# Kernel tuning notes

Measured on AMD Instinct MI355X. Metric: run time of the kernel, lower is better.

The kernel has to match this reference:

```python
import jax, jax.numpy as jnp
import numpy as np

N_HEADS = 8
D_MODEL = 512
HEAD_DIM = D_MODEL // N_HEADS


def setup_inputs() -> dict:
    key = jax.random.key(0)
    ks = jax.random.split(key, 9)
    B, T1, T2, D = 1, 4096, 4096, D_MODEL
    w_scale = 0.02
    return {
        "query": jax.random.normal(ks[0], (B, T1, D), dtype=jnp.float32),
        "key": jax.random.normal(ks[1], (B, T2, D), dtype=jnp.float32),
        "value": jax.random.normal(ks[2], (B, T2, D), dtype=jnp.float32),
        # True = padded (masked out); ~half positions masked
        "key_padding_mask": jax.random.randint(ks[3], (B, T2), 0, 2) == 1,
        "Wq_w": jax.random.normal(ks[4], (D, D), dtype=jnp.float32) * w_scale,
        "Wq_b": jnp.zeros((D,), dtype=jnp.float32),
        "Wk_w": jax.random.normal(ks[5], (D, D), dtype=jnp.float32) * w_scale,
        "Wk_b": jnp.zeros((D,), dtype=jnp.float32),
        "Wv_w": jax.random.normal(ks[6], (D, D), dtype=jnp.float32) * w_scale,
        "Wv_b": jnp.zeros((D,), dtype=jnp.float32),
        "Wo_w": jax.random.normal(ks[7], (D, D), dtype=jnp.float32) * w_scale,
        "Wo_b": jnp.zeros((D,), dtype=jnp.float32),
    }


def reference(query, key, value, key_padding_mask,
              Wq_w, Wq_b, Wk_w, Wk_b, Wv_w, Wv_b, Wo_w, Wo_b):
    B, T1, D = query.shape
    T2 = key.shape[1]
    H, HD = N_HEADS, HEAD_DIM

    # torch Linear: y = x @ W.T + b
    q = (query @ Wq_w.T + Wq_b).reshape(B, T1, H, HD).transpose(0, 2, 1, 3)  # [B,H,T1,HD]
    k = (key @ Wk_w.T + Wk_b).reshape(B, T2, H, HD).transpose(0, 2, 1, 3)    # [B,H,T2,HD]
    v = (value @ Wv_w.T + Wv_b).reshape(B, T2, H, HD).transpose(0, 2, 1, 3)  # [B,H,T2,HD]

    scale = 1.0 / (HD ** 0.5)
    scores = jnp.einsum("bhqd,bhkd->bhqk", q, k) * scale                     # [B,H,T1,T2]
    mask_value = jnp.finfo(scores.dtype).min
    scores = jnp.where(key_padding_mask[:, None, None, :], mask_value, scores)

    attn = jax.nn.softmax(scores, axis=-1)                                   # [B,H,T1,T2]
    # dropout p=0.0 (inference) -> identity

    out = jnp.einsum("bhqk,bhkd->bhqd", attn, v)                             # [B,H,T1,HD]
    out = out.transpose(0, 2, 1, 3).reshape(B, T1, D)
    out = out @ Wo_w.T + Wo_b
    return (out, attn)
```

## Files before the change

### kernel.cpp

```cpp
#include <hip/hip_runtime.h>
#include <hip/hip_bf16.h>
#include <float.h>
#include <stdint.h>

typedef __bf16 bf16x8 __attribute__((ext_vector_type(8)));
typedef __bf16 bf16x4 __attribute__((ext_vector_type(4)));
typedef float  f32x4  __attribute__((ext_vector_type(4)));

#define T_SEQ 4096
#define DMODEL 512
#define NH 8
#define HDIM 64
#define KS1 4
#define L2E 1.44269504088896340736f

__device__ __forceinline__ float fexp2(float x) { return __builtin_amdgcn_exp2f(x); }

__device__ __forceinline__ void gl_lds16(const __bf16* g, char* l) {
    __builtin_amdgcn_global_load_lds(
        (const __attribute__((address_space(1))) unsigned int*)(g),
        (__attribute__((address_space(3))) unsigned int*)(l),
        16, 0, 0);
}

__global__ __launch_bounds__(256) void qkv_kernel(
    const float* __restrict__ qin, const float* __restrict__ kin, const float* __restrict__ vin,
    const float* __restrict__ Wq, const float* __restrict__ bq,
    const float* __restrict__ Wk, const float* __restrict__ bk,
    const float* __restrict__ Wv, const float* __restrict__ bv,
    __bf16* __restrict__ qo, __bf16* __restrict__ ko, __bf16* __restrict__ vt)
{
    __shared__ char lds[16384];
    char* Ab = lds;
    char* Bb = lds + 8192;

    const int z = blockIdx.z;
    const float* X    = (z == 0) ? qin : (z == 1) ? kin : vin;
    const float* W    = (z == 0) ? Wq  : (z == 1) ? Wk  : Wv;
    const float* bias = (z == 0) ? bq  : (z == 1) ? bk  : bv;

    const int m0 = blockIdx.x * 64;
    const int n0 = blockIdx.y * 64;
    const int tid  = threadIdx.x;
    const int w    = tid >> 6;
    const int lane = tid & 63;
    const int lrow = lane & 15;
    const int lgrp = lane >> 4;

    f32x4 acc[4] = {};
    const int r  = tid >> 2;
    const int c0 = (tid & 3) * 16;

    for (int kt = 0; kt < 8; ++kt) {
        const int k0 = kt * 64;
        const float* gA = X + (size_t)(m0 + r) * DMODEL + k0 + c0;
        const float* gB = W + (size_t)(n0 + r) * DMODEL + k0 + c0;
        const int sw = (r & 7) << 4;
#pragma unroll
        for (int i = 0; i < 4; ++i) {
            float4 a4 = *(const float4*)(gA + 4 * i);
            float4 b4 = *(const float4*)(gB + 4 * i);
            bf16x4 av, bv4;
            av[0] = (__bf16)a4.x; av[1] = (__bf16)a4.y; av[2] = (__bf16)a4.z; av[3] = (__bf16)a4.w;
            bv4[0] = (__bf16)b4.x; bv4[1] = (__bf16)b4.y; bv4[2] = (__bf16)b4.z; bv4[3] = (__bf16)b4.w;
            *(bf16x4*)(Ab + r * 128 + ((c0 * 2 + 8 * i) ^ sw)) = av;
            *(bf16x4*)(Bb + r * 128 + ((c0 * 2 + 8 * i) ^ sw)) = bv4;
        }
        __syncthreads();
#pragma unroll
        for (int ks = 0; ks < 2; ++ks) {
            bf16x8 af = *(const bf16x8*)(Ab + (w * 16 + lrow) * 128 +
                                         ((ks * 64 + lgrp * 16) ^ ((lrow & 7) << 4)));
#pragma unroll
            for (int ns = 0; ns < 4; ++ns) {
                bf16x8 bf = *(const bf16x8*)(Bb + (ns * 16 + lrow) * 128 +
                                             ((ks * 64 + lgrp * 16) ^ ((lrow & 7) << 4)));
                acc[ns] = __builtin_amdgcn_mfma_f32_16x16x32_bf16(af, bf, acc[ns], 0, 0, 0);
            }
        }
        __syncthreads();
    }

    if (z == 2) {
        char* LT = lds;
#pragma unroll
        for (int ns = 0; ns < 4; ++ns) {
            float bcol = bias[n0 + ns * 16 + lrow];
#pragma unroll
            for (int rr = 0; rr < 4; ++rr) {
                int col = ns * 16 + lrow;
                int row = w * 16 + lgrp * 4 + rr;
                *(__bf16*)(LT + col * 128 + ((row * 2) ^ ((col & 7) << 4))) =
                    (__bf16)(acc[ns][rr] + bcol);
            }
        }
        __syncthreads();
        int d  = tid >> 2;
        int nb = (tid & 3) * 32;
        bf16x8 t0 = *(const bf16x8*)(LT + d * 128 + (nb ^ ((d & 7) << 4)));
        bf16x8 t1 = *(const bf16x8*)(LT + d * 128 + ((nb + 16) ^ ((d & 7) << 4)));
        __bf16* dst = vt + (size_t)(n0 + d) * T_SEQ + m0 + (tid & 3) * 16;
        *(bf16x8*)dst = t0;
        *(bf16x8*)(dst + 8) = t1;
    } else {
        __bf16* out = (z == 0) ? qo : ko;
        const float sc = (z == 0) ? 0.125f : 1.0f;
#pragma unroll
        for (int ns = 0; ns < 4; ++ns) {
            float bcol = bias[n0 + ns * 16 + lrow];
#pragma unroll
            for (int rr = 0; rr < 4; ++rr) {
                int orow = m0 + w * 16 + lgrp * 4 + rr;
                out[(size_t)orow * DMODEL + n0 + ns * 16 + lrow] =
                    (__bf16)((acc[ns][rr] + bcol) * sc);
            }
        }
    }
}

__global__ __launch_bounds__(256) void attn_stats(
    const __bf16* __restrict__ qb, const __bf16* __restrict__ kb,
    const int* __restrict__ mask, float* __restrict__ l_part)
{
    __shared__ char lds[16384];
    char* KB0 = lds;
    char* KB1 = lds + 8192;

    const int b    = blockIdx.x;
    const int rmap = (b & 7) * ((64 * NH * KS1) / 8) + (b >> 3);
    const int qbi  = rmap & 63;
    const int h    = (rmap >> 6) & (NH - 1);
    const int ksp  = rmap >> 9;
    const int q0   = qbi * 64;
    const int k0   = ksp * (T_SEQ / KS1);

    const int tid  = threadIdx.x;
    const int w    = tid >> 6;
    const int lane = tid & 63;
    const int lrow = lane & 15;
    const int lgrp = lane >> 4;
    const int swl  = (lrow & 7) << 4;

    bf16x8 qa[2];
    {
        const __bf16* qp = qb + (size_t)(q0 + w * 16 + lrow) * DMODEL + h * HDIM;
        qa[0] = *(const bf16x8*)(qp + lgrp * 8);
        qa[1] = *(const bf16x8*)(qp + 32 + lgrp * 8);
    }

    const int key0 = w * 16 + (lane >> 3);
    const int key1 = key0 + 8;
    const int g    = lane & 7;
    const __bf16* sK0 = kb + (size_t)(k0 + key0) * DMODEL + h * HDIM + (g ^ (key0 & 7)) * 8;
    const __bf16* sK1 = kb + (size_t)(k0 + key1) * DMODEL + h * HDIM + (g ^ (key1 & 7)) * 8;

    float lsum[4] = {0.f, 0.f, 0.f, 0.f};

    gl_lds16(sK0, KB0 + w * 2048);
    gl_lds16(sK1, KB0 + w * 2048 + 1024);
    __syncthreads();

    char* cur = KB0;
    char* nxt = KB1;
    const int NT = (T_SEQ / KS1) / 64;
    for (int kt = 0; kt < NT; ++kt) {
        if (kt + 1 < NT) {
            gl_lds16(sK0 + (size_t)(kt + 1) * 64 * DMODEL, nxt + w * 2048);
            gl_lds16(sK1 + (size_t)(kt + 1) * 64 * DMODEL, nxt + w * 2048 + 1024);
        }
        float bias[4][4];
#pragma unroll
        for (int ns = 0; ns < 4; ++ns) {
            int4 mi = *(const int4*)(mask + k0 + kt * 64 + ns * 16 + lgrp * 4);
            bias[ns][0] = mi.x ? -1e30f : 0.f;
            bias[ns][1] = mi.y ? -1e30f : 0.f;
            bias[ns][2] = mi.z ? -1e30f : 0.f;
            bias[ns][3] = mi.w ? -1e30f : 0.f;
        }

        f32x4 acc[4] = {};
        __builtin_amdgcn_s_setprio(1);
#pragma unroll
        for (int ns = 0; ns < 4; ++ns) {
            bf16x8 kf0 = *(const bf16x8*)(cur + (ns * 16 + lrow) * 128 + ((lgrp * 16) ^ swl));
            bf16x8 kf1 = *(const bf16x8*)(cur + (ns * 16 + lrow) * 128 + ((64 + lgrp * 16) ^ swl));
            acc[ns] = __builtin_amdgcn_mfma_f32_16x16x32_bf16(kf0, qa[0], acc[ns], 0, 0, 0);
            acc[ns] = __builtin_amdgcn_mfma_f32_16x16x32_bf16(kf1, qa[1], acc[ns], 0, 0, 0);
        }
        __builtin_amdgcn_s_setprio(0);
#pragma unroll
        for (int ns = 0; ns < 4; ++ns)
#pragma unroll
            for (int rr = 0; rr < 4; ++rr)
                lsum[ns] += fexp2(fmaf(acc[ns][rr], L2E, bias[ns][rr]));
        __syncthreads();
        char* t = cur; cur = nxt; nxt = t;
    }

    float tot = (lsum[0] + lsum[1]) + (lsum[2] + lsum[3]);
    tot += __shfl_xor(tot, 16);
    tot += __shfl_xor(tot, 32);
    if (lgrp == 0)
        l_part[((size_t)h * KS1 + ksp) * T_SEQ + q0 + w * 16 + lrow] = tot;
}

__global__ __launch_bounds__(256) void attn_main(
    const __bf16* __restrict__ qb, const __bf16* __restrict__ kb,
    const __bf16* __restrict__ vt, const int* __restrict__ mask,
    const float* __restrict__ l_part,
    float* __restrict__ attn_out, void* __restrict__ opart,
    int KSP2, int of32)
{
    __shared__ char lds[61440];
    char* PB = lds + 49152;
    char* MB = lds + 57344;

    const int nwg  = 64 * NH * KSP2;
    const int b    = blockIdx.x;
    const int rmap = (b & 7) * (nwg >> 3) + (b >> 3);
    const int qbi  = rmap & 63;
    const int h    = (rmap >> 6) & (NH - 1);
    const int kz   = rmap >> 9;
    const int q0   = qbi * 64;
    const int kspan = T_SEQ / KSP2;
    const int k0   = kz * kspan;
    const int NT   = kspan / 64;

    const int tid  = threadIdx.x;
    const int w    = tid >> 6;
    const int lane = tid & 63;
    const int lrow = lane & 15;
    const int lgrp = lane >> 4;
    const int swl  = (lrow & 7) << 4;

    bf16x8 qa[2];
    {
        const __bf16* qp = qb + (size_t)(q0 + w * 16 + lrow) * DMODEL + h * HDIM;
        qa[0] = *(const bf16x8*)(qp + lgrp * 8);
        qa[1] = *(const bf16x8*)(qp + 32 + lgrp * 8);
    }

    float rl;
    {
        float s = 0.f;
#pragma unroll
        for (int ks = 0; ks < KS1; ++ks)
            s += l_part[((size_t)h * KS1 + ks) * T_SEQ + q0 + w * 16 + lrow];
        rl = 1.0f / s;
    }

    {
        int4 mi = *(const int4*)(mask + k0 + tid * 4);
        f32x4 mb;
        mb[0] = mi.x ? -1e30f : 0.f;
        mb[1] = mi.y ? -1e30f : 0.f;
        mb[2] = mi.z ? -1e30f : 0.f;
        mb[3] = mi.w ? -1e30f : 0.f;
        *(f32x4*)(MB + tid * 16) = mb;
    }

    const int key0 = w * 16 + (lane >> 3);
    const int key1 = key0 + 8;
    const int g    = lane & 7;
    const __bf16* sK0 = kb + (size_t)(k0 + key0) * DMODEL + h * HDIM + (g ^ (key0 & 7)) * 8;
    const __bf16* sK1 = kb + (size_t)(k0 + key1) * DMODEL + h * HDIM + (g ^ (key1 & 7)) * 8;
    const __bf16* sV0 = vt + (size_t)(h * HDIM + key0) * T_SEQ + k0 + (g ^ (key0 & 7)) * 8;
    const __bf16* sV1 = vt + (size_t)(h * HDIM + key1) * T_SEQ + k0 + (g ^ (key1 & 7)) * 8;

#define STAGE(tt, buf) do {                                             \
        size_t koff_ = (size_t)(tt) * 64 * DMODEL;                      \
        size_t voff_ = (size_t)(tt) * 64;                               \
        gl_lds16(sK0 + koff_, (buf) + w * 2048);                        \
        gl_lds16(sK1 + koff_, (buf) + w * 2048 + 1024);                 \
        gl_lds16(sV0 + voff_, (buf) + 8192 + w * 2048);                 \
        gl_lds16(sV1 + voff_, (buf) + 8192 + w * 2048 + 1024);          \
    } while (0)

    f32x4 oacc[4] = {};
    float* arow = attn_out + (size_t)h * T_SEQ * T_SEQ +
                  (size_t)(q0 + w * 16 + lrow) * T_SEQ + k0 + lgrp * 4;
    char* Pw = PB + w * 2048;

    char* bA = lds;
    char* bB = lds + 16384;
    char* bC = lds + 32768;

    STAGE(0, bA);
    STAGE(1, bB);
    __syncthreads();

    for (int kt = 0; kt < NT; ++kt) {
        if (kt + 2 < NT) STAGE(kt + 2, bC);
        __builtin_amdgcn_sched_barrier(0);

        f32x4 acc[4] = {};
        __builtin_amdgcn_s_setprio(1);
#pragma unroll
        for (int ns = 0; ns < 4; ++ns) {
            bf16x8 kf0 = *(const bf16x8*)(bA + (ns * 16 + lrow) * 128 + ((lgrp * 16) ^ swl));
            bf16x8 kf1 = *(const bf16x8*)(bA + (ns * 16 + lrow) * 128 + ((64 + lgrp * 16) ^ swl));
            acc[ns] = __builtin_amdgcn_mfma_f32_16x16x32_bf16(kf0, qa[0], acc[ns], 0, 0, 0);
            acc[ns] = __builtin_amdgcn_mfma_f32_16x16x32_bf16(kf1, qa[1], acc[ns], 0, 0, 0);
        }
        __builtin_amdgcn_s_setprio(0);

#pragma unroll
        for (int ns = 0; ns < 4; ++ns) {
            f32x4 mb = *(const f32x4*)(MB + ((kt * 64 + ns * 16 + lgrp * 4) << 2));
            f32x4 pv;
#pragma unroll
            for (int rr = 0; rr < 4; ++rr)
                pv[rr] = fexp2(fmaf(acc[ns][rr], L2E, mb[rr])) * rl;
            bf16x4 pb;
            pb[0] = (__bf16)pv[0]; pb[1] = (__bf16)pv[1];
            pb[2] = (__bf16)pv[2]; pb[3] = (__bf16)pv[3];
            *(bf16x4*)(Pw + lrow * 128 + ((ns * 32 + lgrp * 8) ^ swl)) = pb;
            *(f32x4*)(arow + kt * 64 + ns * 16) = pv;
        }

        __builtin_amdgcn_s_setprio(1);
#pragma unroll
        for (int ks = 0; ks < 2; ++ks) {
            bf16x8 pa = *(const bf16x8*)(Pw + lrow * 128 + ((ks * 64 + lgrp * 16) ^ swl));
#pragma unroll
            for (int dsb = 0; dsb < 4; ++dsb) {
                bf16x8 vf = *(const bf16x8*)(bA + 8192 + (dsb * 16 + lrow) * 128 +
                                             ((ks * 64 + lgrp * 16) ^ swl));
                oacc[dsb] = __builtin_amdgcn_mfma_f32_16x16x32_bf16(vf, pa, oacc[dsb], 0, 0, 0);
            }
        }
        __builtin_amdgcn_s_setprio(0);

        if (kt + 1 < NT) {
            if (kt == NT - 2) asm volatile("s_waitcnt vmcnt(8)" ::: "memory");
            else              asm volatile("s_waitcnt vmcnt(12)" ::: "memory");
            __builtin_amdgcn_s_barrier();
            __builtin_amdgcn_sched_barrier(0);
        }
        char* tmp = bA; bA = bB; bB = bC; bC = tmp;
    }
#undef STAGE

    if (of32) {
        float* op = (float*)opart + (size_t)kz * T_SEQ * DMODEL +
                    (size_t)(q0 + w * 16 + lrow) * DMODEL + h * HDIM + lgrp * 4;
#pragma unroll
        for (int dsb = 0; dsb < 4; ++dsb)
            *(f32x4*)(op + dsb * 16) = oacc[dsb];
    } else {
        __bf16* op = (__bf16*)opart + (size_t)(q0 + w * 16 + lrow) * DMODEL + h * HDIM + lgrp * 4;
#pragma unroll
        for (int dsb = 0; dsb < 4; ++dsb) {
            bf16x4 ob;
            ob[0] = (__bf16)oacc[dsb][0]; ob[1] = (__bf16)oacc[dsb][1];
            ob[2] = (__bf16)oacc[dsb][2]; ob[3] = (__bf16)oacc[dsb][3];
            *(bf16x4*)(op + dsb * 16) = ob;
        }
    }
}

__global__ __launch_bounds__(256) void oproj_kernel(
    const void* __restrict__ opart, const float* __restrict__ Wo,
    const float* __restrict__ bo, float* __restrict__ out, int KSP2, int of32)
{
    __shared__ char lds[16384];
    char* Ab = lds;
    char* Bb = lds + 8192;

    const int m0 = blockIdx.x * 64;
    const int n0 = blockIdx.y * 64;
    const int tid  = threadIdx.x;
    const int w    = tid >> 6;
    const int lane = tid & 63;
    const int lrow = lane & 15;
    const int lgrp = lane >> 4;

    f32x4 acc[4] = {};
    const int r   = tid >> 2;
    const int c0e = (tid & 3) * 16;
    const int sw  = (r & 7) << 4;

    for (int kt = 0; kt < 8; ++kt) {
        const int k0 = kt * 64;
        if (of32) {
            const float* p0 = (const float*)opart + (size_t)(m0 + r) * DMODEL + k0 + c0e;
#pragma unroll
            for (int i = 0; i < 4; ++i) {
                f32x4 a4 = *(const f32x4*)(p0 + 4 * i);
                for (int s = 1; s < KSP2; ++s)
                    a4 = a4 + *(const f32x4*)(p0 + (size_t)s * T_SEQ * DMODEL + 4 * i);
                bf16x4 av;
                av[0] = (__bf16)a4[0]; av[1] = (__bf16)a4[1];
                av[2] = (__bf16)a4[2]; av[3] = (__bf16)a4[3];
                *(bf16x4*)(Ab + r * 128 + ((c0e * 2 + 8 * i) ^ sw)) = av;
            }
        } else {
            const __bf16* pa = (const __bf16*)opart + (size_t)(m0 + r) * DMODEL + k0 + c0e;
            bf16x8 a0 = *(const bf16x8*)pa;
            bf16x8 a1 = *(const bf16x8*)(pa + 8);
            *(bf16x8*)(Ab + r * 128 + ((c0e * 2) ^ sw)) = a0;
            *(bf16x8*)(Ab + r * 128 + ((c0e * 2 + 16) ^ sw)) = a1;
        }
        const float* gB = Wo + (size_t)(n0 + r) * DMODEL + k0 + c0e;
#pragma unroll
        for (int i = 0; i < 4; ++i) {
            float4 b4 = *(const float4*)(gB + 4 * i);
            bf16x4 bv4;
            bv4[0] = (__bf16)b4.x; bv4[1] = (__bf16)b4.y;
            bv4[2] = (__bf16)b4.z; bv4[3] = (__bf16)b4.w;
            *(bf16x4*)(Bb + r * 128 + ((c0e * 2 + 8 * i) ^ sw)) = bv4;
        }
        __syncthreads();
#pragma unroll
        for (int ks = 0; ks < 2; ++ks) {
            bf16x8 af = *(const bf16x8*)(Ab + (w * 16 + lrow) * 128 +
                                         ((ks * 64 + lgrp * 16) ^ ((lrow & 7) << 4)));
#pragma unroll
            for (int ns = 0; ns < 4; ++ns) {
                bf16x8 bf = *(const bf16x8*)(Bb + (ns * 16 + lrow) * 128 +
                                             ((ks * 64 + lgrp * 16) ^ ((lrow & 7) << 4)));
                acc[ns] = __builtin_amdgcn_mfma_f32_16x16x32_bf16(af, bf, acc[ns], 0, 0, 0);
            }
        }
        __syncthreads();
    }

#pragma unroll
    for (int ns = 0; ns < 4; ++ns) {
        float bcol = bo[n0 + ns * 16 + lrow];
#pragma unroll
        for (int rr = 0; rr < 4; ++rr) {
            int orow = m0 + w * 16 + lgrp * 4 + rr;
            out[(size_t)orow * DMODEL + n0 + ns * 16 + lrow] = acc[ns][rr] + bcol;
        }
    }
}

extern "C" void kernel_launch(void* const* d_in, const int* in_sizes, int n_in,
                              void* d_out, int out_size, void* d_ws, size_t ws_size,
                              hipStream_t stream) {
    const float* query = (const float*)d_in[0];
    const float* key   = (const float*)d_in[1];
    const float* value = (const float*)d_in[2];
    const int*   mask  = (const int*)d_in[3];
    const float* Wq = (const float*)d_in[4];
    const float* bq = (const float*)d_in[5];
    const float* Wk = (const float*)d_in[6];
    const float* bk = (const float*)d_in[7];
    const float* Wv = (const float*)d_in[8];
    const float* bv = (const float*)d_in[9];
    const float* Wo = (const float*)d_in[10];
    const float* bo = (const float*)d_in[11];

    float* out  = (float*)d_out;
    float* attn = out + (size_t)T_SEQ * DMODEL;

    char* ws = (char*)d_ws;
    __bf16* qo     = (__bf16*)(ws);
    __bf16* ko     = (__bf16*)(ws + (4u << 20));
    __bf16* vt     = (__bf16*)(ws + (8u << 20));
    float*  l_part = (float*)(ws + (12u << 20));
    void*   opart  = (void*)(ws + (12u << 20) + (1u << 19));
    const size_t obase = (12u << 20) + (1u << 19);

    int KSP2, of32;
    const size_t oslice = (size_t)T_SEQ * DMODEL * 4;
    if (ws_size >= obase + 4 * oslice)      { KSP2 = 4; of32 = 1; }
    else if (ws_size >= obase + 2 * oslice) { KSP2 = 2; of32 = 1; }
    else if (ws_size >= obase + oslice)     { KSP2 = 1; of32 = 1; }
    else                                    { KSP2 = 1; of32 = 0; }

    qkv_kernel<<<dim3(64, 8, 3), 256, 0, stream>>>(query, key, value,
                                                   Wq, bq, Wk, bk, Wv, bv, qo, ko, vt);
    attn_stats<<<dim3(64 * NH * KS1), 256, 0, stream>>>(qo, ko, mask, l_part);
    attn_main<<<dim3(64 * NH * KSP2), 256, 0, stream>>>(qo, ko, vt, mask, l_part,
                                                        attn, opart, KSP2, of32);
    oproj_kernel<<<dim3(64, 8), 256, 0, stream>>>(opart, Wo, bo, out, KSP2, of32);
}
```

Baseline: 268.2 us.

## Shrink LDS to double buffering and split P staging into halves

```diff
diff --git a/kernel.cpp b/kernel.cpp
--- a/kernel.cpp
+++ b/kernel.cpp
@@ -211,9 +211,9 @@
     float* __restrict__ attn_out, void* __restrict__ opart,
     int KSP2, int of32)
 {
-    __shared__ char lds[61440];
-    char* PB = lds + 49152;
-    char* MB = lds + 57344;
+    __shared__ char lds[40960];
+    char* PB = lds + 32768;
+    char* MB = lds + 36864;
 
     const int nwg  = 64 * NH * KSP2;
     const int b    = blockIdx.x;
@@ -225,6 +225,7 @@
     const int kspan = T_SEQ / KSP2;
     const int k0   = kz * kspan;
     const int NT   = kspan / 64;
+    const bool mlds = (kspan <= 1024);
 
     const int tid  = threadIdx.x;
     const int w    = tid >> 6;
@@ -232,6 +233,7 @@
     const int lrow = lane & 15;
     const int lgrp = lane >> 4;
     const int swl  = (lrow & 7) << 4;
+    const int swp  = (lrow & 3) << 4;
 
     bf16x8 qa[2];
     {
@@ -249,7 +251,7 @@
         rl = 1.0f / s;
     }
 
-    {
+    if (mlds) {
         int4 mi = *(const int4*)(mask + k0 + tid * 4);
         f32x4 mb;
         mb[0] = mi.x ? -1e30f : 0.f;
@@ -279,18 +281,16 @@
     f32x4 oacc[4] = {};
     float* arow = attn_out + (size_t)h * T_SEQ * T_SEQ +
                   (size_t)(q0 + w * 16 + lrow) * T_SEQ + k0 + lgrp * 4;
-    char* Pw = PB + w * 2048;
+    char* Pw = PB + w * 1024;
 
     char* bA = lds;
     char* bB = lds + 16384;
-    char* bC = lds + 32768;
 
     STAGE(0, bA);
-    STAGE(1, bB);
     __syncthreads();
 
     for (int kt = 0; kt < NT; ++kt) {
-        if (kt + 2 < NT) STAGE(kt + 2, bC);
+        if (kt + 1 < NT) STAGE(kt + 1, bB);
         __builtin_amdgcn_sched_barrier(0);
 
         f32x4 acc[4] = {};
@@ -304,40 +304,60 @@
         }
         __builtin_amdgcn_s_setprio(0);
 
-#pragma unroll
-        for (int ns = 0; ns < 4; ++ns) {
-            f32x4 mb = *(const f32x4*)(MB + ((kt * 64 + ns * 16 + lgrp * 4) << 2));
-            f32x4 pv;
-#pragma unroll
-            for (int rr = 0; rr < 4; ++rr)
-                pv[rr] = fexp2(fmaf(acc[ns][rr], L2E, mb[rr])) * rl;
-            bf16x4 pb;
-            pb[0] = (__bf16)pv[0]; pb[1] = (__bf16)pv[1];
-            pb[2] = (__bf16)pv[2]; pb[3] = (__bf16)pv[3];
-            *(bf16x4*)(Pw + lrow * 128 + ((ns * 32 + lgrp * 8) ^ swl)) = pb;
-            *(f32x4*)(arow + kt * 64 + ns * 16) = pv;
-        }
-
-        __builtin_amdgcn_s_setprio(1);
-#pragma unroll
-        for (int ks = 0; ks < 2; ++ks) {
-            bf16x8 pa = *(const bf16x8*)(Pw + lrow * 128 + ((ks * 64 + lgrp * 16) ^ swl));
-#pragma unroll
-            for (int dsb = 0; dsb < 4; ++dsb) {
-                bf16x8 vf = *(const bf16x8*)(bA + 8192 + (dsb * 16 + lrow) * 128 +
-                                             ((ks * 64 + lgrp * 16) ^ swl));
-                oacc[dsb] = __builtin_amdgcn_mfma_f32_16x16x32_bf16(vf, pa, oacc[dsb], 0, 0, 0);
-            }
-        }
-        __builtin_amdgcn_s_setprio(0);
+        f32x4 mb[4];
+        if (mlds) {
+#pragma unroll
+            for (int ns = 0; ns < 4; ++ns)
+                mb[ns] = *(const f32x4*)(MB + ((kt * 64 + ns * 16 + lgrp * 4) << 2));
+        } else {
+#pragma unroll
+            for (int ns = 0; ns < 4; ++ns) {
+                int4 mi = *(const int4*)(mask + k0 + kt * 64 + ns * 16 + lgrp * 4);
+                mb[ns][0] = mi.x ? -1e30f : 0.f;
+                mb[ns][1] = mi.y ? -1e30f : 0.f;
+                mb[ns][2] = mi.z ? -1e30f : 0.f;
+                mb[ns][3] = mi.w ? -1e30f : 0.f;
+            }
+        }
+
+#pragma unroll
+        for (int half = 0; half < 2; ++half) {
+#pragma unroll
+            for (int nsl = 0; nsl < 2; ++nsl) {
+                int ns = half * 2 + nsl;
+                f32x4 pv;
+#pragma unroll
+                for (int rr = 0; rr < 4; ++rr)
+                    pv[rr] = fexp2(fmaf(acc[ns][rr], L2E, mb[ns][rr])) * rl;
+                bf16x4 pb;
+                pb[0] = (__bf16)pv[0]; pb[1] = (__bf16)pv[1];
+                pb[2] = (__bf16)pv[2]; pb[3] = (__bf16)pv[3];
+                *(bf16x4*)(Pw + lrow * 64 + ((nsl * 32 + lgrp * 8) ^ swp)) = pb;
+                *(f32x4*)(arow + kt * 64 + ns * 16) = pv;
+            }
+            __builtin_amdgcn_s_setprio(1);
+            {
+                bf16x8 pa = *(const bf16x8*)(Pw + lrow * 64 + ((lgrp * 16) ^ swp));
+#pragma unroll
+                for (int dsb = 0; dsb < 4; ++dsb) {
+                    bf16x8 vf = *(const bf16x8*)(bA + 8192 + (dsb * 16 + lrow) * 128 +
+                                                 ((half * 64 + lgrp * 16) ^ swl));
+                    oacc[dsb] = __builtin_amdgcn_mfma_f32_16x16x32_bf16(vf, pa, oacc[dsb], 0, 0, 0);
+                }
+            }
+            __builtin_amdgcn_s_setprio(0);
+        }
 
         if (kt + 1 < NT) {
-            if (kt == NT - 2) asm volatile("s_waitcnt vmcnt(8)" ::: "memory");
-            else              asm volatile("s_waitcnt vmcnt(12)" ::: "memory");
-            __builtin_amdgcn_s_barrier();
-            __builtin_amdgcn_sched_barrier(0);
-        }
-        char* tmp = bA; bA = bB; bB = bC; bC = tmp;
+            if (mlds) {
+                asm volatile("s_waitcnt vmcnt(4)" ::: "memory");
+                __builtin_amdgcn_s_barrier();
+                __builtin_amdgcn_sched_barrier(0);
+            } else {
+                __syncthreads();
+            }
+        }
+        char* tmp = bA; bA = bB; bB = tmp;
     }
 #undef STAGE
 
```

Measured after the change: 261.1 us. 2.6% less time.

## Load K/V fragments directly from global memory and double per-wave query rows

Applied to the files above, without the earlier changes.

```diff
diff --git a/kernel.cpp b/kernel.cpp
--- a/kernel.cpp
+++ b/kernel.cpp
@@ -15,13 +15,6 @@
 #define L2E 1.44269504088896340736f
 
 __device__ __forceinline__ float fexp2(float x) { return __builtin_amdgcn_exp2f(x); }
-
-__device__ __forceinline__ void gl_lds16(const __bf16* g, char* l) {
-    __builtin_amdgcn_global_load_lds(
-        (const __attribute__((address_space(1))) unsigned int*)(g),
-        (__attribute__((address_space(3))) unsigned int*)(l),
-        16, 0, 0);
-}
 
 __global__ __launch_bounds__(256) void qkv_kernel(
     const float* __restrict__ qin, const float* __restrict__ kin, const float* __restrict__ vin,
@@ -118,21 +111,98 @@
     }
 }
 
-__global__ __launch_bounds__(256) void attn_stats(
+__global__ __launch_bounds__(256, 3) void attn_stats(
     const __bf16* __restrict__ qb, const __bf16* __restrict__ kb,
     const int* __restrict__ mask, float* __restrict__ l_part)
 {
-    __shared__ char lds[16384];
-    char* KB0 = lds;
-    char* KB1 = lds + 8192;
-
+    const int nwg  = 32 * NH * KS1;
     const int b    = blockIdx.x;
-    const int rmap = (b & 7) * ((64 * NH * KS1) / 8) + (b >> 3);
-    const int qbi  = rmap & 63;
-    const int h    = (rmap >> 6) & (NH - 1);
-    const int ksp  = rmap >> 9;
-    const int q0   = qbi * 64;
+    const int rmap = (b & 7) * (nwg >> 3) + (b >> 3);
+    const int qsi  = rmap & 31;
+    const int h    = (rmap >> 5) & (NH - 1);
+    const int ksp  = rmap >> 8;
+    const int q0   = qsi * 128;
     const int k0   = ksp * (T_SEQ / KS1);
+
+    const int tid  = threadIdx.x;
+    const int w    = tid >> 6;
+    const int lane = tid & 63;
+    const int lrow = lane & 15;
+    const int lgrp = lane >> 4;
+    const int q0w  = q0 + w * 32;
+
+    bf16x8 qa[2][2];
+#pragma unroll
+    for (int q2 = 0; q2 < 2; ++q2) {
+        const __bf16* qp = qb + (size_t)(q0w + q2 * 16 + lrow) * DMODEL + h * HDIM;
+        qa[q2][0] = *(const bf16x8*)(qp + lgrp * 8);
+        qa[q2][1] = *(const bf16x8*)(qp + 32 + lgrp * 8);
+    }
+
+    const __bf16* kbase = kb + (size_t)(k0 + lrow) * DMODEL + h * HDIM + lgrp * 8;
+
+    float lsum[2][4] = {};
+    const int NT = (T_SEQ / KS1) / 64;
+
+    for (int kt = 0; kt < NT; ++kt) {
+        f32x4 acc[2][4] = {};
+        __builtin_amdgcn_s_setprio(1);
+#pragma unroll
+        for (int ns = 0; ns < 4; ++ns) {
+            const __bf16* kp = kbase + (size_t)(kt * 64 + ns * 16) * DMODEL;
+            bf16x8 kf0 = *(const bf16x8*)(kp);
+            bf16x8 kf1 = *(const bf16x8*)(kp + 32);
+            acc[0][ns] = __builtin_amdgcn_mfma_f32_16x16x32_bf16(kf0, qa[0][0], acc[0][ns], 0, 0, 0);
+            acc[0][ns] = __builtin_amdgcn_mfma_f32_16x16x32_bf16(kf1, qa[0][1], acc[0][ns], 0, 0, 0);
+            acc[1][ns] = __builtin_amdgcn_mfma_f32_16x16x32_bf16(kf0, qa[1][0], acc[1][ns], 0, 0, 0);
+            acc[1][ns] = __builtin_amdgcn_mfma_f32_16x16x32_bf16(kf1, qa[1][1], acc[1][ns], 0, 0, 0);
+        }
+        __builtin_amdgcn_s_setprio(0);
+#pragma unroll
+        for (int ns = 0; ns < 4; ++ns) {
+            int4 mi = *(const int4*)(mask + k0 + kt * 64 + ns * 16 + lgrp * 4);
+            f32x4 mb;
+            mb[0] = mi.x ? -1e30f : 0.f;
+            mb[1] = mi.y ? -1e30f : 0.f;
+            mb[2] = mi.z ? -1e30f : 0.f;
+            mb[3] = mi.w ? -1e30f : 0.f;
+#pragma unroll
+            for (int q2 = 0; q2 < 2; ++q2)
+#pragma unroll
+                for (int rr = 0; rr < 4; ++rr)
+                    lsum[q2][ns] += fexp2(fmaf(acc[q2][ns][rr], L2E, mb[rr]));
+        }
+    }
+
+#pragma unroll
+    for (int q2 = 0; q2 < 2; ++q2) {
+        float tot = (lsum[q2][0] + lsum[q2][1]) + (lsum[q2][2] + lsum[q2][3]);
+        tot += __shfl_xor(tot, 16);
+        tot += __shfl_xor(tot, 32);
+        if (lgrp == 0)
+            l_part[((size_t)h * KS1 + ksp) * T_SEQ + q0w + q2 * 16 + lrow] = tot;
+    }
+}
+
+__global__ __launch_bounds__(256, 3) void attn_main(
+    const __bf16* __restrict__ qb, const __bf16* __restrict__ kb,
+    const __bf16* __restrict__ vt, const int* __restrict__ mask,
+    const float* __restrict__ l_part,
+    float* __restrict__ attn_out, void* __restrict__ opart,
+    int KSP2, int of32)
+{
+    __shared__ char PB[16384];
+
+    const int nwg  = 32 * NH * KSP2;
+    const int b    = blockIdx.x;
+    const int rmap = (b & 7) * (nwg >> 3) + (b >> 3);
+    const int qsi  = rmap & 31;
+    const int h    = (rmap >> 5) & (NH - 1);
+    const int kz   = rmap >> 8;
+    const int q0   = qsi * 128;
+    const int kspan = T_SEQ / KSP2;
+    const int k0   = kz * kspan;
+    const int NT   = kspan / 64;
 
     const int tid  = threadIdx.x;
     const int w    = tid >> 6;
@@ -140,221 +210,108 @@
     const int lrow = lane & 15;
     const int lgrp = lane >> 4;
     const int swl  = (lrow & 7) << 4;
-
-    bf16x8 qa[2];
-    {
-        const __bf16* qp = qb + (size_t)(q0 + w * 16 + lrow) * DMODEL + h * HDIM;
-        qa[0] = *(const bf16x8*)(qp + lgrp * 8);
-        qa[1] = *(const bf16x8*)(qp + 32 + lgrp * 8);
-    }
-
-    const int key0 = w * 16 + (lane >> 3);
-    const int key1 = key0 + 8;
-    const int g    = lane & 7;
-    const __bf16* sK0 = kb + (size_t)(k0 + key0) * DMODEL + h * HDIM + (g ^ (key0 & 7)) * 8;
-    const __bf16* sK1 = kb + (size_t)(k0 + key1) * DMODEL + h * HDIM + (g ^ (key1 & 7)) * 8;
-
-    float lsum[4] = {0.f, 0.f, 0.f, 0.f};
-
-    gl_lds16(sK0, KB0 + w * 2048);
-    gl_lds16(sK1, KB0 + w * 2048 + 1024);
-    __syncthreads();
-
-    char* cur = KB0;
-    char* nxt = KB1;
-    const int NT = (T_SEQ / KS1) / 64;
+    const int q0w  = q0 + w * 32;
+
+    bf16x8 qa[2][2];
+#pragma unroll
+    for (int q2 = 0; q2 < 2; ++q2) {
+        const __bf16* qp = qb + (size_t)(q0w + q2 * 16 + lrow) * DMODEL + h * HDIM;
+        qa[q2][0] = *(const bf16x8*)(qp + lgrp * 8);
+        qa[q2][1] = *(const bf16x8*)(qp + 32 + lgrp * 8);
+    }
+
+    float rl[2];
+#pragma unroll
+    for (int q2 = 0; q2 < 2; ++q2) {
+        float s = 0.f;
+#pragma unroll
+        for (int ks = 0; ks < KS1; ++ks)
+            s += l_part[((size_t)h * KS1 + ks) * T_SEQ + q0w + q2 * 16 + lrow];
+        rl[q2] = 1.0f / s;
+    }
+
+    const __bf16* kbase = kb + (size_t)(k0 + lrow) * DMODEL + h * HDIM + lgrp * 8;
+    const __bf16* vbase = vt + (size_t)(h * HDIM + lrow) * T_SEQ + k0 + lgrp * 8;
+    float* arow = attn_out + (size_t)h * T_SEQ * T_SEQ +
+                  (size_t)(q0w + lrow) * T_SEQ + k0 + lgrp * 4;
+    char* Pw = PB + w * 4096;
+
+    f32x4 oacc[2][4] = {};
+
     for (int kt = 0; kt < NT; ++kt) {
-        if (kt + 1 < NT) {
-            gl_lds16(sK0 + (size_t)(kt + 1) * 64 * DMODEL, nxt + w * 2048);
-            gl_lds16(sK1 + (size_t)(kt + 1) * 64 * DMODEL, nxt + w * 2048 + 1024);
-        }
-        float bias[4][4];
+        f32x4 acc[2][4] = {};
+        __builtin_amdgcn_s_setprio(1);
+#pragma unroll
+        for (int ns = 0; ns < 4; ++ns) {
+            const __bf16* kp = kbase + (size_t)(kt * 64 + ns * 16) * DMODEL;
+            bf16x8 kf0 = *(const bf16x8*)(kp);
+            bf16x8 kf1 = *(const bf16x8*)(kp + 32);
+            acc[0][ns] = __builtin_amdgcn_mfma_f32_16x16x32_bf16(kf0, qa[0][0], acc[0][ns], 0, 0, 0);
+            acc[0][ns] = __builtin_amdgcn_mfma_f32_16x16x32_bf16(kf1, qa[0][1], acc[0][ns], 0, 0, 0);
+            acc[1][ns] = __builtin_amdgcn_mfma_f32_16x16x32_bf16(kf0, qa[1][0], acc[1][ns], 0, 0, 0);
+            acc[1][ns] = __builtin_amdgcn_mfma_f32_16x16x32_bf16(kf1, qa[1][1], acc[1][ns], 0, 0, 0);
+        }
+        __builtin_amdgcn_s_setprio(0);
+
 #pragma unroll
         for (int ns = 0; ns < 4; ++ns) {
             int4 mi = *(const int4*)(mask + k0 + kt * 64 + ns * 16 + lgrp * 4);
-            bias[ns][0] = mi.x ? -1e30f : 0.f;
-            bias[ns][1] = mi.y ? -1e30f : 0.f;
-            bias[ns][2] = mi.z ? -1e30f : 0.f;
-            bias[ns][3] = mi.w ? -1e30f : 0.f;
-        }
-
-        f32x4 acc[4] = {};
+            f32x4 mb;
+            mb[0] = mi.x ? -1e30f : 0.f;
+            mb[1] = mi.y ? -1e30f : 0.f;
+            mb[2] = mi.z ? -1e30f : 0.f;
+            mb[3] = mi.w ? -1e30f : 0.f;
+#pragma unroll
+            for (int q2 = 0; q2 < 2; ++q2) {
+                f32x4 pv;
+#pragma unroll
+                for (int rr = 0; rr < 4; ++rr)
+                    pv[rr] = fexp2(fmaf(acc[q2][ns][rr], L2E, mb[rr])) * rl[q2];
+                bf16x4 pb;
+                pb[0] = (__bf16)pv[0]; pb[1] = (__bf16)pv[1];
+                pb[2] = (__bf16)pv[2]; pb[3] = (__bf16)pv[3];
+                *(bf16x4*)(Pw + (q2 * 16 + lrow) * 128 + ((ns * 32 + lgrp * 8) ^ swl)) = pb;
+                *(f32x4*)(arow + (size_t)(q2 * 16) * T_SEQ + kt * 64 + ns * 16) = pv;
+            }
+        }
+
         __builtin_amdgcn_s_setprio(1);
 #pragma unroll
-        for (int ns = 0; ns < 4; ++ns) {
-            bf16x8 kf0 = *(const bf16x8*)(cur + (ns * 16 + lrow) * 128 + ((lgrp * 16) ^ swl));
-            bf16x8 kf1 = *(const bf16x8*)(cur + (ns * 16 + lrow) * 128 + ((64 + lgrp * 16) ^ swl));
-            acc[ns] = __builtin_amdgcn_mfma_f32_16x16x32_bf16(kf0, qa[0], acc[ns], 0, 0, 0);
-            acc[ns] = __builtin_amdgcn_mfma_f32_16x16x32_bf16(kf1, qa[1], acc[ns], 0, 0, 0);
+        for (int ks = 0; ks < 2; ++ks) {
+            bf16x8 pa0 = *(const bf16x8*)(Pw + lrow * 128 + ((ks * 64 + lgrp * 16) ^ swl));
+            bf16x8 pa1 = *(const bf16x8*)(Pw + (16 + lrow) * 128 + ((ks * 64 + lgrp * 16) ^ swl));
+#pragma unroll
+            for (int dsb = 0; dsb < 4; ++dsb) {
+                bf16x8 vf = *(const bf16x8*)(vbase + (size_t)(dsb * 16) * T_SEQ +
+                                             kt * 64 + ks * 32);
+                oacc[0][dsb] = __builtin_amdgcn_mfma_f32_16x16x32_bf16(vf, pa0, oacc[0][dsb], 0, 0, 0);
+                oacc[1][dsb] = __builtin_amdgcn_mfma_f32_16x16x32_bf16(vf, pa1, oacc[1][dsb], 0, 0, 0);
+            }
         }
         __builtin_amdgcn_s_setprio(0);
-#pragma unroll
-        for (int ns = 0; ns < 4; ++ns)
-#pragma unroll
-            for (int rr = 0; rr < 4; ++rr)
-                lsum[ns] += fexp2(fmaf(acc[ns][rr], L2E, bias[ns][rr]));
-        __syncthreads();
-        char* t = cur; cur = nxt; nxt = t;
-    }
-
-    float tot = (lsum[0] + lsum[1]) + (lsum[2] + lsum[3]);
-    tot += __shfl_xor(tot, 16);
-    tot += __shfl_xor(tot, 32);
-    if (lgrp == 0)
-        l_part[((size_t)h * KS1 + ksp) * T_SEQ + q0 + w * 16 + lrow] = tot;
-}
-
-__global__ __launch_bounds__(256) void attn_main(
-    const __bf16* __restrict__ qb, const __bf16* __restrict__ kb,
-    const __bf16* __restrict__ vt, const int* __restrict__ mask,
-    const float* __restrict__ l_part,
-    float* __restrict__ attn_out, void* __restrict__ opart,
-    int KSP2, int of32)
-{
-    __shared__ char lds[61440];
-    char* PB = lds + 49152;
-    char* MB = lds + 57344;
-
-    const int nwg  = 64 * NH * KSP2;
-    const int b    = blockIdx.x;
-    const int rmap = (b & 7) * (nwg >> 3) + (b >> 3);
-    const int qbi  = rmap & 63;
-    const int h    = (rmap >> 6) & (NH - 1);
-    const int kz   = rmap >> 9;
-    const int q0   = qbi * 64;
-    const int kspan = T_SEQ / KSP2;
-    const int k0   = kz * kspan;
-    const int NT   = kspan / 64;
-
-    const int tid  = threadIdx.x;
-    const int w    = tid >> 6;
-    const int lane = tid & 63;
-    const int lrow = lane & 15;
-    const int lgrp = lane >> 4;
-    const int swl  = (lrow & 7) << 4;
-
-    bf16x8 qa[2];
-    {
-        const __bf16* qp = qb + (size_t)(q0 + w * 16 + lrow) * DMODEL + h * HDIM;
-        qa[0] = *(const bf16x8*)(qp + lgrp * 8);
-        qa[1] = *(const bf16x8*)(qp + 32 + lgrp * 8);
-    }
-
-    float rl;
-    {
-        float s = 0.f;
-#pragma unroll
-        for (int ks = 0; ks < KS1; ++ks)
-            s += l_part[((size_t)h * KS1 + ks) * T_SEQ + q0 + w * 16 + lrow];
-        rl = 1.0f / s;
-    }
-
-    {
-        int4 mi = *(const int4*)(mask + k0 + tid * 4);
-        f32x4 mb;
-        mb[0] = mi.x ? -1e30f : 0.f;
-        mb[1] = mi.y ? -1e30f : 0.f;
-        mb[2] = mi.z ? -1e30f : 0.f;
-        mb[3] = mi.w ? -1e30f : 0.f;
-        *(f32x4*)(MB + tid * 16) = mb;
-    }
-
-    const int key0 = w * 16 + (lane >> 3);
-    const int key1 = key0 + 8;
-    const int g    = lane & 7;
-    const __bf16* sK0 = kb + (size_t)(k0 + key0) * DMODEL + h * HDIM + (g ^ (key0 & 7)) * 8;
-    const __bf16* sK1 = kb + (size_t)(k0 + key1) * DMODEL + h * HDIM + (g ^ (key1 & 7)) * 8;
-    const __bf16* sV0 = vt + (size_t)(h * HDIM + key0) * T_SEQ + k0 + (g ^ (key0 & 7)) * 8;
-    const __bf16* sV1 = vt + (size_t)(h * HDIM + key1) * T_SEQ + k0 + (g ^ (key1 & 7)) * 8;
-
-#define STAGE(tt, buf) do {                                             \
-        size_t koff_ = (size_t)(tt) * 64 * DMODEL;                      \
-        size_t voff_ = (size_t)(tt) * 64;                               \
-        gl_lds16(sK0 + koff_, (buf) + w * 2048);                        \
-        gl_lds16(sK1 + koff_, (buf) + w * 2048 + 1024);                 \
-        gl_lds16(sV0 + voff_, (buf) + 8192 + w * 2048);                 \
-        gl_lds16(sV1 + voff_, (buf) + 8192 + w * 2048 + 1024);          \
-    } while (0)
-
-    f32x4 oacc[4] = {};
-    float* arow = attn_out + (size_t)h * T_SEQ * T_SEQ +
-                  (size_t)(q0 + w * 16 + lrow) * T_SEQ + k0 + lgrp * 4;
-    char* Pw = PB + w * 2048;
-
-    char* bA = lds;
-    char* bB = lds + 16384;
-    char* bC = lds + 32768;
-
-    STAGE(0, bA);
-    STAGE(1, bB);
-    __syncthreads();
-
-    for (int kt = 0; kt < NT; ++kt) {
-        if (kt + 2 < NT) STAGE(kt + 2, bC);
-        __builtin_amdgcn_sched_barrier(0);
-
-        f32x4 acc[4] = {};
-        __builtin_amdgcn_s_setprio(1);
-#pragma unroll
-        for (int ns = 0; ns < 4; ++ns) {
-            bf16x8 kf0 = *(const bf16x8*)(bA + (ns * 16 + lrow) * 128 + ((lgrp * 16) ^ swl));
-            bf16x8 kf1 = *(const bf16x8*)(bA + (ns * 16 + lrow) * 128 + ((64 + lgrp * 16) ^ swl));
-            acc[ns] = __builtin_amdgcn_mfma_f32_16x16x32_bf16(kf0, qa[0], acc[ns], 0, 0, 0);
-            acc[ns] = __builtin_amdgcn_mfma_f32_16x16x32_bf16(kf1, qa[1], acc[ns], 0, 0, 0);
-        }
-        __builtin_amdgcn_s_setprio(0);
-
-#pragma unroll
-        for (int ns = 0; ns < 4; ++ns) {
-            f32x4 mb = *(const f32x4*)(MB + ((kt * 64 + ns * 16 + lgrp * 4) << 2));
-            f32x4 pv;
-#pragma unroll
-            for (int rr = 0; rr < 4; ++rr)
-                pv[rr] = fexp2(fmaf(acc[ns][rr], L2E, mb[rr])) * rl;
-            bf16x4 pb;
-            pb[0] = (__bf16)pv[0]; pb[1] = (__bf16)pv[1];
-            pb[2] = (__bf16)pv[2]; pb[3] = (__bf16)pv[3];
-            *(bf16x4*)(Pw + lrow * 128 + ((ns * 32 + lgrp * 8) ^ swl)) = pb;
-            *(f32x4*)(arow + kt * 64 + ns * 16) = pv;
-        }
-
-        __builtin_amdgcn_s_setprio(1);
-#pragma unroll
-        for (int ks = 0; ks < 2; ++ks) {
-            bf16x8 pa = *(const bf16x8*)(Pw + lrow * 128 + ((ks * 64 + lgrp * 16) ^ swl));
+    }
+
+    if (of32) {
+        float* op = (float*)opart + (size_t)kz * T_SEQ * DMODEL;
+#pragma unroll
+        for (int q2 = 0; q2 < 2; ++q2) {
+            float* oq = op + (size_t)(q0w + q2 * 16 + lrow) * DMODEL + h * HDIM + lgrp * 4;
+#pragma unroll
+            for (int dsb = 0; dsb < 4; ++dsb)
+                *(f32x4*)(oq + dsb * 16) = oacc[q2][dsb];
+        }
+    } else {
+        __bf16* op = (__bf16*)opart;
+#pragma unroll
+        for (int q2 = 0; q2 < 2; ++q2) {
+            __bf16* oq = op + (size_t)(q0w + q2 * 16 + lrow) * DMODEL + h * HDIM + lgrp * 4;
 #pragma unroll
             for (int dsb = 0; dsb < 4; ++dsb) {
-                bf16x8 vf = *(const bf16x8*)(bA + 8192 + (dsb * 16 + lrow) * 128 +
-                                             ((ks * 64 + lgrp * 16) ^ swl));
-                oacc[dsb] = __builtin_amdgcn_mfma_f32_16x16x32_bf16(vf, pa, oacc[dsb], 0, 0, 0);
-            }
-        }
-        __builtin_amdgcn_s_setprio(0);
-
-        if (kt + 1 < NT) {
-            if (kt == NT - 2) asm volatile("s_waitcnt vmcnt(8)" ::: "memory");
-            else              asm volatile("s_waitcnt vmcnt(12)" ::: "memory");
-            __builtin_amdgcn_s_barrier();
-            __builtin_amdgcn_sched_barrier(0);
-        }
-        char* tmp = bA; bA = bB; bB = bC; bC = tmp;
-    }
-#undef STAGE
-
-    if (of32) {
-        float* op = (float*)opart + (size_t)kz * T_SEQ * DMODEL +
-                    (size_t)(q0 + w * 16 + lrow) * DMODEL + h * HDIM + lgrp * 4;
-#pragma unroll
-        for (int dsb = 0; dsb < 4; ++dsb)
-            *(f32x4*)(op + dsb * 16) = oacc[dsb];
-    } else {
-        __bf16* op = (__bf16*)opart + (size_t)(q0 + w * 16 + lrow) * DMODEL + h * HDIM + lgrp * 4;
-#pragma unroll
-        for (int dsb = 0; dsb < 4; ++dsb) {
-            bf16x4 ob;
-            ob[0] = (__bf16)oacc[dsb][0]; ob[1] = (__bf16)oacc[dsb][1];
-            ob[2] = (__bf16)oacc[dsb][2]; ob[3] = (__bf16)oacc[dsb][3];
-            *(bf16x4*)(op + dsb * 16) = ob;
+                bf16x4 ob;
+                ob[0] = (__bf16)oacc[q2][dsb][0]; ob[1] = (__bf16)oacc[q2][dsb][1];
+                ob[2] = (__bf16)oacc[q2][dsb][2]; ob[3] = (__bf16)oacc[q2][dsb][3];
+                *(bf16x4*)(oq + dsb * 16) = ob;
+            }
         }
     }
 }
@@ -472,8 +429,8 @@
 
     qkv_kernel<<<dim3(64, 8, 3), 256, 0, stream>>>(query, key, value,
                                                    Wq, bq, Wk, bk, Wv, bv, qo, ko, vt);
-    attn_stats<<<dim3(64 * NH * KS1), 256, 0, stream>>>(qo, ko, mask, l_part);
-    attn_main<<<dim3(64 * NH * KSP2), 256, 0, stream>>>(qo, ko, vt, mask, l_part,
+    attn_stats<<<dim3(32 * NH * KS1), 256, 0, stream>>>(qo, ko, mask, l_part);
+    attn_main<<<dim3(32 * NH * KSP2), 256, 0, stream>>>(qo, ko, vt, mask, l_part,
                                                         attn, opart, KSP2, of32);
     oproj_kernel<<<dim3(64, 8), 256, 0, stream>>>(opart, Wo, bo, out, KSP2, of32);
 }
```

Result: slower. 495.6 us (+84.8%).

## Widen stats tile to 128 queries, simplify attn_main to double buffering

Applied to the files above, without the earlier changes.

```diff
diff --git a/kernel.cpp b/kernel.cpp
--- a/kernel.cpp
+++ b/kernel.cpp
@@ -126,12 +126,13 @@
     char* KB0 = lds;
     char* KB1 = lds + 8192;
 
+    const int nwg  = 32 * NH * KS1;
     const int b    = blockIdx.x;
-    const int rmap = (b & 7) * ((64 * NH * KS1) / 8) + (b >> 3);
-    const int qbi  = rmap & 63;
-    const int h    = (rmap >> 6) & (NH - 1);
-    const int ksp  = rmap >> 9;
-    const int q0   = qbi * 64;
+    const int rmap = (b & 7) * (nwg >> 3) + (b >> 3);
+    const int qsi  = rmap & 31;
+    const int h    = (rmap >> 5) & (NH - 1);
+    const int ksp  = rmap >> 8;
+    const int q0   = qsi * 128;
     const int k0   = ksp * (T_SEQ / KS1);
 
     const int tid  = threadIdx.x;
@@ -140,12 +141,14 @@
     const int lrow = lane & 15;
     const int lgrp = lane >> 4;
     const int swl  = (lrow & 7) << 4;
-
-    bf16x8 qa[2];
-    {
-        const __bf16* qp = qb + (size_t)(q0 + w * 16 + lrow) * DMODEL + h * HDIM;
-        qa[0] = *(const bf16x8*)(qp + lgrp * 8);
-        qa[1] = *(const bf16x8*)(qp + 32 + lgrp * 8);
+    const int q0w  = q0 + w * 32;
+
+    bf16x8 qa[2][2];
+#pragma unroll
+    for (int q2 = 0; q2 < 2; ++q2) {
+        const __bf16* qp = qb + (size_t)(q0w + q2 * 16 + lrow) * DMODEL + h * HDIM;
+        qa[q2][0] = *(const bf16x8*)(qp + lgrp * 8);
+        qa[q2][1] = *(const bf16x8*)(qp + 32 + lgrp * 8);
     }
 
     const int key0 = w * 16 + (lane >> 3);
@@ -154,7 +157,7 @@
     const __bf16* sK0 = kb + (size_t)(k0 + key0) * DMODEL + h * HDIM + (g ^ (key0 & 7)) * 8;
     const __bf16* sK1 = kb + (size_t)(k0 + key1) * DMODEL + h * HDIM + (g ^ (key1 & 7)) * 8;
 
-    float lsum[4] = {0.f, 0.f, 0.f, 0.f};
+    float lsum[2][4] = {};
 
     gl_lds16(sK0, KB0 + w * 2048);
     gl_lds16(sK1, KB0 + w * 2048 + 1024);
@@ -168,40 +171,46 @@
             gl_lds16(sK0 + (size_t)(kt + 1) * 64 * DMODEL, nxt + w * 2048);
             gl_lds16(sK1 + (size_t)(kt + 1) * 64 * DMODEL, nxt + w * 2048 + 1024);
         }
-        float bias[4][4];
-#pragma unroll
-        for (int ns = 0; ns < 4; ++ns) {
-            int4 mi = *(const int4*)(mask + k0 + kt * 64 + ns * 16 + lgrp * 4);
-            bias[ns][0] = mi.x ? -1e30f : 0.f;
-            bias[ns][1] = mi.y ? -1e30f : 0.f;
-            bias[ns][2] = mi.z ? -1e30f : 0.f;
-            bias[ns][3] = mi.w ? -1e30f : 0.f;
-        }
-
-        f32x4 acc[4] = {};
+
+        f32x4 acc[2][4] = {};
         __builtin_amdgcn_s_setprio(1);
 #pragma unroll
         for (int ns = 0; ns < 4; ++ns) {
             bf16x8 kf0 = *(const bf16x8*)(cur + (ns * 16 + lrow) * 128 + ((lgrp * 16) ^ swl));
             bf16x8 kf1 = *(const bf16x8*)(cur + (ns * 16 + lrow) * 128 + ((64 + lgrp * 16) ^ swl));
-            acc[ns] = __builtin_amdgcn_mfma_f32_16x16x32_bf16(kf0, qa[0], acc[ns], 0, 0, 0);
-            acc[ns] = __builtin_amdgcn_mfma_f32_16x16x32_bf16(kf1, qa[1], acc[ns], 0, 0, 0);
+            acc[0][ns] = __builtin_amdgcn_mfma_f32_16x16x32_bf16(kf0, qa[0][0], acc[0][ns], 0, 0, 0);
+            acc[0][ns] = __builtin_amdgcn_mfma_f32_16x16x32_bf16(kf1, qa[0][1], acc[0][ns], 0, 0, 0);
+            acc[1][ns] = __builtin_amdgcn_mfma_f32_16x16x32_bf16(kf0, qa[1][0], acc[1][ns], 0, 0, 0);
+            acc[1][ns] = __builtin_amdgcn_mfma_f32_16x16x32_bf16(kf1, qa[1][1], acc[1][ns], 0, 0, 0);
         }
         __builtin_amdgcn_s_setprio(0);
-#pragma unroll
-        for (int ns = 0; ns < 4; ++ns)
-#pragma unroll
-            for (int rr = 0; rr < 4; ++rr)
-                lsum[ns] += fexp2(fmaf(acc[ns][rr], L2E, bias[ns][rr]));
+
+#pragma unroll
+        for (int ns = 0; ns < 4; ++ns) {
+            int4 mi = *(const int4*)(mask + k0 + kt * 64 + ns * 16 + lgrp * 4);
+            f32x4 mb;
+            mb[0] = mi.x ? -1e30f : 0.f;
+            mb[1] = mi.y ? -1e30f : 0.f;
+            mb[2] = mi.z ? -1e30f : 0.f;
+            mb[3] = mi.w ? -1e30f : 0.f;
+#pragma unroll
+            for (int q2 = 0; q2 < 2; ++q2)
+#pragma unroll
+                for (int rr = 0; rr < 4; ++rr)
+                    lsum[q2][ns] += fexp2(fmaf(acc[q2][ns][rr], L2E, mb[rr]));
+        }
         __syncthreads();
         char* t = cur; cur = nxt; nxt = t;
     }
 
-    float tot = (lsum[0] + lsum[1]) + (lsum[2] + lsum[3]);
-    tot += __shfl_xor(tot, 16);
-    tot += __shfl_xor(tot, 32);
-    if (lgrp == 0)
-        l_part[((size_t)h * KS1 + ksp) * T_SEQ + q0 + w * 16 + lrow] = tot;
+#pragma unroll
+    for (int q2 = 0; q2 < 2; ++q2) {
+        float tot = (lsum[q2][0] + lsum[q2][1]) + (lsum[q2][2] + lsum[q2][3]);
+        tot += __shfl_xor(tot, 16);
+        tot += __shfl_xor(tot, 32);
+        if (lgrp == 0)
+            l_part[((size_t)h * KS1 + ksp) * T_SEQ + q0w + q2 * 16 + lrow] = tot;
+    }
 }
 
 __global__ __launch_bounds__(256) void attn_main(
@@ -211,9 +220,8 @@
     float* __restrict__ attn_out, void* __restrict__ opart,
     int KSP2, int of32)
 {
-    __shared__ char lds[61440];
-    char* PB = lds + 49152;
-    char* MB = lds + 57344;
+    __shared__ char lds[40960];
+    char* PB  = lds + 32768;
 
     const int nwg  = 64 * NH * KSP2;
     const int b    = blockIdx.x;
@@ -249,16 +257,6 @@
         rl = 1.0f / s;
     }
 
-    {
-        int4 mi = *(const int4*)(mask + k0 + tid * 4);
-        f32x4 mb;
-        mb[0] = mi.x ? -1e30f : 0.f;
-        mb[1] = mi.y ? -1e30f : 0.f;
-        mb[2] = mi.z ? -1e30f : 0.f;
-        mb[3] = mi.w ? -1e30f : 0.f;
-        *(f32x4*)(MB + tid * 16) = mb;
-    }
-
     const int key0 = w * 16 + (lane >> 3);
     const int key1 = key0 + 8;
     const int g    = lane & 7;
@@ -283,15 +281,12 @@
 
     char* bA = lds;
     char* bB = lds + 16384;
-    char* bC = lds + 32768;
 
     STAGE(0, bA);
-    STAGE(1, bB);
     __syncthreads();
 
     for (int kt = 0; kt < NT; ++kt) {
-        if (kt + 2 < NT) STAGE(kt + 2, bC);
-        __builtin_amdgcn_sched_barrier(0);
+        if (kt + 1 < NT) STAGE(kt + 1, bB);
 
         f32x4 acc[4] = {};
         __builtin_amdgcn_s_setprio(1);
@@ -304,18 +299,24 @@
         }
         __builtin_amdgcn_s_setprio(0);
 
-#pragma unroll
-        for (int ns = 0; ns < 4; ++ns) {
-            f32x4 mb = *(const f32x4*)(MB + ((kt * 64 + ns * 16 + lgrp * 4) << 2));
+        f32x4 pvs[4];
+#pragma unroll
+        for (int ns = 0; ns < 4; ++ns) {
+            int4 mi = *(const int4*)(mask + k0 + kt * 64 + ns * 16 + lgrp * 4);
+            f32x4 mb;
+            mb[0] = mi.x ? -1e30f : 0.f;
+            mb[1] = mi.y ? -1e30f : 0.f;
+            mb[2] = mi.z ? -1e30f : 0.f;
+            mb[3] = mi.w ? -1e30f : 0.f;
             f32x4 pv;
 #pragma unroll
             for (int rr = 0; rr < 4; ++rr)
                 pv[rr] = fexp2(fmaf(acc[ns][rr], L2E, mb[rr])) * rl;
+            pvs[ns] = pv;
             bf16x4 pb;
             pb[0] = (__bf16)pv[0]; pb[1] = (__bf16)pv[1];
             pb[2] = (__bf16)pv[2]; pb[3] = (__bf16)pv[3];
             *(bf16x4*)(Pw + lrow * 128 + ((ns * 32 + lgrp * 8) ^ swl)) = pb;
-            *(f32x4*)(arow + kt * 64 + ns * 16) = pv;
         }
 
         __builtin_amdgcn_s_setprio(1);
@@ -331,13 +332,12 @@
         }
         __builtin_amdgcn_s_setprio(0);
 
-        if (kt + 1 < NT) {
-            if (kt == NT - 2) asm volatile("s_waitcnt vmcnt(8)" ::: "memory");
-            else              asm volatile("s_waitcnt vmcnt(12)" ::: "memory");
-            __builtin_amdgcn_s_barrier();
-            __builtin_amdgcn_sched_barrier(0);
-        }
-        char* tmp = bA; bA = bB; bB = bC; bC = tmp;
+#pragma unroll
+        for (int ns = 0; ns < 4; ++ns)
+            *(f32x4*)(arow + kt * 64 + ns * 16) = pvs[ns];
+
+        __syncthreads();
+        char* tmp = bA; bA = bB; bB = tmp;
     }
 #undef STAGE
 
@@ -465,14 +465,13 @@
 
     int KSP2, of32;
     const size_t oslice = (size_t)T_SEQ * DMODEL * 4;
-    if (ws_size >= obase + 4 * oslice)      { KSP2 = 4; of32 = 1; }
-    else if (ws_size >= obase + 2 * oslice) { KSP2 = 2; of32 = 1; }
+    if (ws_size >= obase + 2 * oslice)      { KSP2 = 2; of32 = 1; }
     else if (ws_size >= obase + oslice)     { KSP2 = 1; of32 = 1; }
     else                                    { KSP2 = 1; of32 = 0; }
 
     qkv_kernel<<<dim3(64, 8, 3), 256, 0, stream>>>(query, key, value,
                                                    Wq, bq, Wk, bk, Wv, bv, qo, ko, vt);
-    attn_stats<<<dim3(64 * NH * KS1), 256, 0, stream>>>(qo, ko, mask, l_part);
+    attn_stats<<<dim3(32 * NH * KS1), 256, 0, stream>>>(qo, ko, mask, l_part);
     attn_main<<<dim3(64 * NH * KSP2), 256, 0, stream>>>(qo, ko, vt, mask, l_part,
                                                         attn, opart, KSP2, of32);
     oproj_kernel<<<dim3(64, 8), 256, 0, stream>>>(opart, Wo, bo, out, KSP2, of32);
```

New measurement: 233.5 us. -13.0%, faster.
